# Performance work log

Measured on AMD Instinct MI355X. Metric: run time of the kernel, lower is better.

## Reference

```python
import jax, jax.numpy as jnp
import numpy as np

EMBED_DIM = 768
NUM_HEADS = 8
HEAD_DIM = EMBED_DIM // NUM_HEADS
SCALE = HEAD_DIM ** -0.5
B = 256
N_TOTAL = 16384


def setup_inputs() -> dict:
    key = jax.random.key(0)
    ks = jax.random.split(key, 10)
    s = 1.0 / np.sqrt(EMBED_DIM)
    inp = {
        "query": jax.random.normal(ks[0], (B, EMBED_DIM), jnp.float32),
        "search": jax.random.normal(ks[1], (N_TOTAL, EMBED_DIM), jnp.float32),
        # q_proj / k_proj: Linear(embed_dim, embed_dim)
        "Wq": jax.random.uniform(ks[2], (EMBED_DIM, EMBED_DIM), jnp.float32, -s, s),
        "bq": jax.random.uniform(ks[3], (EMBED_DIM,), jnp.float32, -s, s),
        "Wk": jax.random.uniform(ks[4], (EMBED_DIM, EMBED_DIM), jnp.float32, -s, s),
        "bk": jax.random.uniform(ks[5], (EMBED_DIM,), jnp.float32, -s, s),
        # score_fusion: Linear(H, H//2) -> GELU -> Linear(H//2, 1)
        "W1": jax.random.uniform(ks[6], (NUM_HEADS // 2, NUM_HEADS), jnp.float32, -1.0 / np.sqrt(NUM_HEADS), 1.0 / np.sqrt(NUM_HEADS)),
        "b1": jax.random.uniform(ks[7], (NUM_HEADS // 2,), jnp.float32, -1.0 / np.sqrt(NUM_HEADS), 1.0 / np.sqrt(NUM_HEADS)),
        "W2": jax.random.uniform(ks[8], (1, NUM_HEADS // 2), jnp.float32, -1.0 / np.sqrt(NUM_HEADS // 2), 1.0 / np.sqrt(NUM_HEADS // 2)),
        "b2": jax.random.uniform(ks[9], (1,), jnp.float32, -1.0 / np.sqrt(NUM_HEADS // 2), 1.0 / np.sqrt(NUM_HEADS // 2)),
    }
    return inp


def reference(query, search, Wq, bq, Wk, bk, W1, b1, W2, b2):
    Bq = query.shape[0]
    Nt = search.shape[0]
    # projections -> (B, H, hd) and (N, H, hd)
    q = (query @ Wq.T + bq).reshape(Bq, NUM_HEADS, HEAD_DIM)
    k = (search @ Wk.T + bk).reshape(Nt, NUM_HEADS, HEAD_DIM)
    # per-head dot products: (B, N, H)
    attn_logits = jnp.einsum('bhd,nhd->bnh', q, k) * SCALE
    # tiny MLP over head axis: H -> H//2 -> 1, exact (erf) GELU as in torch default
    h = jax.nn.gelu(attn_logits @ W1.T + b1, approximate=False)
    scores = h @ W2.T + b2  # (B, N, 1)
    return scores.squeeze(-1)
```

## Files before the change

### kernel.cpp

```cpp
#include <hip/hip_runtime.h>
#include <math.h>

#define SCALE 0.1020620726159658f

typedef __attribute__((ext_vector_type(8))) short shortx8;
typedef __attribute__((ext_vector_type(4))) float floatx4;

__device__ __forceinline__ unsigned short f2bf(float f) {
  union { float f; unsigned int i; } c; c.f = f;
  unsigned int x = c.i;
  x += 0x7fffu + ((x >> 16) & 1u);
  return (unsigned short)(x >> 16);
}
__device__ __forceinline__ float gelu_fast(float x) {
  float x2 = x * x;
  float y = x * (0.7978845608f + 0.0356774081f * x2);
  float e = fminf(y * 2.885390082f, 60.0f);
  float t = exp2f(e);
  return x * t * __builtin_amdgcn_rcpf(t + 1.0f);
}
__device__ __forceinline__ void async_ld16(const unsigned short* g, unsigned short* l) {
  __builtin_amdgcn_global_load_lds(
      (const __attribute__((address_space(1))) unsigned int*)g,
      (__attribute__((address_space(3))) unsigned int*)l, 16, 0, 0);
}
__device__ __forceinline__ void cvt_store8(const float* __restrict__ src,
                                           unsigned short* __restrict__ dst) {
  float4 a = *(const float4*)src;
  float4 b = *(const float4*)(src + 4);
  shortx8 v;
  v[0] = (short)f2bf(a.x); v[1] = (short)f2bf(a.y);
  v[2] = (short)f2bf(a.z); v[3] = (short)f2bf(a.w);
  v[4] = (short)f2bf(b.x); v[5] = (short)f2bf(b.y);
  v[6] = (short)f2bf(b.z); v[7] = (short)f2bf(b.w);
  *(shortx8*)dst = v;
}
__device__ __forceinline__ void mfma_consume(const unsigned short* __restrict__ As,
                                             const unsigned short* __restrict__ Bs,
                                             int wr, int wc, int quad, int l15,
                                             floatx4 (&acc)[4][4]) {
#pragma unroll
  for (int ks = 0; ks < 2; ks++) {
    shortx8 af[4], bfr[4];
#pragma unroll
    for (int mt = 0; mt < 4; mt++) {
      int r = wr * 64 + mt * 16 + l15;
      int ch = (ks * 4 + quad) ^ (r & 7);
      af[mt] = *(const shortx8*)(As + r * 64 + ch * 8);
    }
#pragma unroll
    for (int nt = 0; nt < 4; nt++) {
      int r = wc * 64 + nt * 16 + l15;
      int ch = (ks * 4 + quad) ^ (r & 7);
      bfr[nt] = *(const shortx8*)(Bs + r * 64 + ch * 8);
    }
#pragma unroll
    for (int mt = 0; mt < 4; mt++)
#pragma unroll
      for (int nt = 0; nt < 4; nt++)
        acc[mt][nt] = __builtin_amdgcn_mfma_f32_16x16x32_bf16(
            af[mt], bfr[nt], acc[mt][nt], 0, 0, 0);
  }
}

__global__ __launch_bounds__(256) void k_pre(
    const float* __restrict__ query, const float* __restrict__ Wq,
    const float* __restrict__ bq, const float* __restrict__ W1,
    const float* __restrict__ Wk, const float* __restrict__ search,
    float* __restrict__ qf, unsigned short* __restrict__ QW,
    unsigned short* __restrict__ WkT, unsigned short* __restrict__ sb,
    int use_sb)
{
  __shared__ unsigned short As[64 * 64];
  __shared__ unsigned short Bs[64 * 64];
  __shared__ unsigned short tile[32][33];
  const int bid = blockIdx.x, t = threadIdx.x;
  const int wave = t >> 6, lane = t & 63;
  if (bid < 48) {
    const int by = bid / 12, bx = bid % 12;
    const int m0 = by * 64, n0 = bx * 64;
    const int wr = wave >> 1, wc = wave & 1;
    const int quad = lane >> 4, l15 = lane & 15;
    const int rl = lane >> 3, cL = lane & 7, p = cL ^ rl;
    floatx4 acc[2][2];
#pragma unroll
    for (int i = 0; i < 2; i++)
#pragma unroll
      for (int j = 0; j < 2; j++) acc[i][j] = (floatx4){0.f, 0.f, 0.f, 0.f};
    for (int k0 = 0; k0 < 768; k0 += 64) {
#pragma unroll
      for (int tt = 0; tt < 2; tt++) {
        int r = wave * 16 + tt * 8 + rl;
        cvt_store8(query + (size_t)(m0 + r) * 768 + k0 + cL * 8, As + r * 64 + p * 8);
        cvt_store8(Wq + (size_t)(n0 + r) * 768 + k0 + cL * 8, Bs + r * 64 + p * 8);
      }
      __syncthreads();
#pragma unroll
      for (int ks = 0; ks < 2; ks++) {
        shortx8 af[2], bfr[2];
#pragma unroll
        for (int mt = 0; mt < 2; mt++) {
          int r = wr * 32 + mt * 16 + l15;
          int ch = (ks * 4 + quad) ^ (r & 7);
          af[mt] = *(const shortx8*)(As + r * 64 + ch * 8);
        }
#pragma unroll
        for (int nt = 0; nt < 2; nt++) {
          int r = wc * 32 + nt * 16 + l15;
          int ch = (ks * 4 + quad) ^ (r & 7);
          bfr[nt] = *(const shortx8*)(Bs + r * 64 + ch * 8);
        }
#pragma unroll
        for (int mt = 0; mt < 2; mt++)
#pragma unroll
          for (int nt = 0; nt < 2; nt++)
            acc[mt][nt] = __builtin_amdgcn_mfma_f32_16x16x32_bf16(
                af[mt], bfr[nt], acc[mt][nt], 0, 0, 0);
      }
      __syncthreads();
    }
    const int lrow = quad * 4;
#pragma unroll
    for (int mt = 0; mt < 2; mt++)
#pragma unroll
      for (int nt = 0; nt < 2; nt++) {
        int gm = m0 + wr * 32 + mt * 16 + lrow;
        int gn = n0 + wc * 32 + nt * 16 + l15;
        float bz = bq[gn];
        int h = gn / 96;
        float w1h0 = W1[h], w1h1 = W1[8 + h], w1h2 = W1[16 + h], w1h3 = W1[24 + h];
#pragma unroll
        for (int r = 0; r < 4; r++) {
          float qv = acc[mt][nt][r] + bz;
          qf[(size_t)(gm + r) * 768 + gn] = qv;
          size_t base = (size_t)((gm + r) * 4) * 768 + gn;
          QW[base]           = f2bf(SCALE * w1h0 * qv);
          QW[base + 768]     = f2bf(SCALE * w1h1 * qv);
          QW[base + 2 * 768] = f2bf(SCALE * w1h2 * qv);
          QW[base + 3 * 768] = f2bf(SCALE * w1h3 * qv);
        }
      }
  } else if (bid < 624) {
    const int tb = bid - 48, bx = tb % 24, by = tb / 24;
    const int tx = t & 31, ty = t >> 5;
#pragma unroll
    for (int i = 0; i < 4; i++)
      tile[ty + i * 8][tx] = f2bf(Wk[(size_t)(by * 32 + ty + i * 8) * 768 + bx * 32 + tx]);
    __syncthreads();
#pragma unroll
    for (int i = 0; i < 4; i++)
      WkT[(size_t)(bx * 32 + ty + i * 8) * 768 + by * 32 + tx] = tile[tx][ty + i * 8];
  } else {
    for (int it = bid - 624; it < 6144; it += 1000) {
      size_t i = (size_t)it * 2048 + t * 8;
      cvt_store8(search + i, sb + i);
    }
  }
}

__global__ __launch_bounds__(256) void k_mid(
    const unsigned short* __restrict__ QW, const unsigned short* __restrict__ WkT,
    unsigned short* __restrict__ QQ,
    const float* __restrict__ qf, const float* __restrict__ W1,
    const float* __restrict__ b1, const float* __restrict__ bk,
    float* __restrict__ cp)
{
  __shared__ unsigned short As[64 * 64];
  __shared__ unsigned short Bs[64 * 64];
  const int bid = blockIdx.x, t = threadIdx.x;
  const int wave = t >> 6, lane = t & 63;
  if (bid < 192) {
    const int by = bid / 12, bx = bid % 12;
    const int m0 = by * 64, n0 = bx * 64;
    const int wr = wave >> 1, wc = wave & 1;
    const int quad = lane >> 4, l15 = lane & 15;
    const int rl = lane >> 3, cl = (lane & 7) ^ rl;
    floatx4 acc[2][2];
#pragma unroll
    for (int i = 0; i < 2; i++)
#pragma unroll
      for (int j = 0; j < 2; j++) acc[i][j] = (floatx4){0.f, 0.f, 0.f, 0.f};
    for (int k0 = 0; k0 < 768; k0 += 64) {
#pragma unroll
      for (int tt = 0; tt < 2; tt++) {
        int rr = wave * 16 + tt * 8;
        async_ld16(QW + (size_t)(m0 + rr + rl) * 768 + k0 + cl * 8, As + rr * 64);
        async_ld16(WkT + (size_t)(n0 + rr + rl) * 768 + k0 + cl * 8, Bs + rr * 64);
      }
      __syncthreads();
#pragma unroll
      for (int ks = 0; ks < 2; ks++) {
        shortx8 af[2], bfr[2];
#pragma unroll
        for (int mt = 0; mt < 2; mt++) {
          int r = wr * 32 + mt * 16 + l15;
          int ch = (ks * 4 + quad) ^ (r & 7);
          af[mt] = *(const shortx8*)(As + r * 64 + ch * 8);
        }
#pragma unroll
        for (int nt = 0; nt < 2; nt++) {
          int r = wc * 32 + nt * 16 + l15;
          int ch = (ks * 4 + quad) ^ (r & 7);
          bfr[nt] = *(const shortx8*)(Bs + r * 64 + ch * 8);
        }
#pragma unroll
        for (int mt = 0; mt < 2; mt++)
#pragma unroll
          for (int nt = 0; nt < 2; nt++)
            acc[mt][nt] = __builtin_amdgcn_mfma_f32_16x16x32_bf16(
                af[mt], bfr[nt], acc[mt][nt], 0, 0, 0);
      }
      __syncthreads();
    }
    const int lrow = quad * 4;
#pragma unroll
    for (int mt = 0; mt < 2; mt++)
#pragma unroll
      for (int nt = 0; nt < 2; nt++) {
        int gm = m0 + wr * 32 + mt * 16 + lrow;
        int gn = n0 + wc * 32 + nt * 16 + l15;
#pragma unroll
        for (int r = 0; r < 4; r++)
          QQ[(size_t)(gm + r) * 768 + gn] = f2bf(acc[mt][nt][r]);
      }
  } else {
    const int bstart = (bid - 192) * 64;
    for (int b = bstart + wave; b < bstart + 64; b += 4) {
      const float* qrow = qf + (size_t)b * 768;
      int e0 = lane * 12;
      float s = 0.f;
#pragma unroll
      for (int i = 0; i < 12; i++) s += qrow[e0 + i] * bk[e0 + i];
      s += __shfl_xor(s, 1); s += __shfl_xor(s, 2); s += __shfl_xor(s, 4);
      float v = __shfl(s, (lane & 7) * 8);
      float w = W1[((lane >> 3) & 3) * 8 + (lane & 7)] * v;
      w += __shfl_xor(w, 1); w += __shfl_xor(w, 2); w += __shfl_xor(w, 4);
      if (lane < 32 && (lane & 7) == 0) {
        int j = lane >> 3;
        cp[b * 4 + j] = b1[j] + SCALE * w;
      }
    }
  }
}

__global__ __launch_bounds__(256) void k_main(
    const unsigned short* __restrict__ QQ, const void* __restrict__ Bv,
    float* __restrict__ out, const float* __restrict__ cp,
    const float* __restrict__ W2, const float* __restrict__ b2, int use_sb)
{
  __shared__ unsigned short As[128 * 64];
  __shared__ unsigned short Bs[128 * 64];
  const int bid = blockIdx.x;
  const int n_tile = (bid & 7) * 16 + ((bid >> 3) & 15);
  const int m_tile = bid >> 7;
  const int m0 = m_tile * 128, n0 = n_tile * 128;
  const int t = threadIdx.x, wave = t >> 6, lane = t & 63;
  const int wr = wave >> 1, wc = wave & 1;
  const int quad = lane >> 4, l15 = lane & 15;
  floatx4 acc[4][4];
#pragma unroll
  for (int i = 0; i < 4; i++)
#pragma unroll
    for (int j = 0; j < 4; j++) acc[i][j] = (floatx4){0.f, 0.f, 0.f, 0.f};
  const int rl = lane >> 3, cl = (lane & 7) ^ rl, cL = lane & 7, p = cL ^ rl;
  for (int k0 = 0; k0 < 768; k0 += 64) {
#pragma unroll
    for (int tt = 0; tt < 4; tt++) {
      int rr = wave * 32 + tt * 8;
      async_ld16(QQ + (size_t)(m0 + rr + rl) * 768 + k0 + cl * 8, As + rr * 64);
    }
    if (use_sb) {
      const unsigned short* B16 = (const unsigned short*)Bv;
#pragma unroll
      for (int tt = 0; tt < 4; tt++) {
        int rr = wave * 32 + tt * 8;
        async_ld16(B16 + (size_t)(n0 + rr + rl) * 768 + k0 + cl * 8, Bs + rr * 64);
      }
    } else {
      const float* Bf = (const float*)Bv;
#pragma unroll
      for (int tt = 0; tt < 4; tt++) {
        int r = wave * 32 + tt * 8 + rl;
        cvt_store8(Bf + (size_t)(n0 + r) * 768 + k0 + cL * 8, Bs + r * 64 + p * 8);
      }
    }
    __syncthreads();
    mfma_consume(As, Bs, wr, wc, quad, l15, acc);
    __syncthreads();
  }
  const float w2v0 = W2[0], w2v1 = W2[1], w2v2 = W2[2], w2v3 = W2[3];
  const float b2v = b2[0];
  const int lrow = quad * 4;
#pragma unroll
  for (int mt = 0; mt < 4; mt++) {
    int gm = m0 + wr * 64 + mt * 16 + lrow;
    float cpv0 = cp[gm], cpv1 = cp[gm + 1], cpv2 = cp[gm + 2], cpv3 = cp[gm + 3];
#pragma unroll
    for (int nt = 0; nt < 4; nt++) {
      int gn = n0 + wc * 64 + nt * 16 + l15;
      floatx4 v = acc[mt][nt];
      float s = b2v;
      s += w2v0 * gelu_fast(v[0] + cpv0);
      s += w2v1 * gelu_fast(v[1] + cpv1);
      s += w2v2 * gelu_fast(v[2] + cpv2);
      s += w2v3 * gelu_fast(v[3] + cpv3);
      out[(size_t)(gm >> 2) * 16384 + gn] = s;
    }
  }
}

extern "C" void kernel_launch(void* const* d_in, const int* in_sizes, int n_in,
                              void* d_out, int out_size, void* d_ws, size_t ws_size,
                              hipStream_t stream) {
  const float* query  = (const float*)d_in[0];
  const float* search = (const float*)d_in[1];
  const float* Wq     = (const float*)d_in[2];
  const float* bq     = (const float*)d_in[3];
  const float* Wk     = (const float*)d_in[4];
  const float* bk     = (const float*)d_in[5];
  const float* W1     = (const float*)d_in[6];
  const float* b1     = (const float*)d_in[7];
  const float* W2     = (const float*)d_in[8];
  const float* b2     = (const float*)d_in[9];
  float* out = (float*)d_out;

  char* ws = (char*)d_ws;
  float*          cp  = (float*)ws;
  float*          qf  = (float*)(ws + 4352);
  unsigned short* WkT = (unsigned short*)(ws + 790784);
  unsigned short* QW  = (unsigned short*)(ws + 1970432);
  unsigned short* QQ  = (unsigned short*)(ws + 3543296);
  unsigned short* sb  = (unsigned short*)(ws + 5116160);
  int use_sb = (ws_size >= 30281984u) ? 1 : 0;

  k_pre<<<use_sb ? 1624 : 624, 256, 0, stream>>>(query, Wq, bq, W1, Wk, search,
                                                 qf, QW, WkT, sb, use_sb);
  k_mid<<<196, 256, 0, stream>>>(QW, WkT, QQ, qf, W1, b1, bk, cp);
  k_main<<<1024, 256, 0, stream>>>(QQ, use_sb ? (const void*)sb : (const void*)search,
                                   out, cp, W2, b2, use_sb);
}
```

Before: 167.9 us.

## Merge mid-stage GEMM into prologue kernel using atomic counter dependency

```diff
diff --git a/kernel.cpp b/kernel.cpp
--- a/kernel.cpp
+++ b/kernel.cpp
@@ -67,9 +67,11 @@
     const float* __restrict__ query, const float* __restrict__ Wq,
     const float* __restrict__ bq, const float* __restrict__ W1,
     const float* __restrict__ Wk, const float* __restrict__ search,
+    const float* __restrict__ b1, const float* __restrict__ bk,
     float* __restrict__ qf, unsigned short* __restrict__ QW,
     unsigned short* __restrict__ WkT, unsigned short* __restrict__ sb,
-    int use_sb)
+    unsigned short* __restrict__ QQ, float* __restrict__ cp,
+    unsigned int* __restrict__ ctr, int use_sb)
 {
   __shared__ unsigned short As[64 * 64];
   __shared__ unsigned short Bs[64 * 64];
@@ -140,6 +142,11 @@
           QW[base + 3 * 768] = f2bf(SCALE * w1h3 * qv);
         }
       }
+    __syncthreads();
+    if (t == 0) {
+      __threadfence();
+      __hip_atomic_fetch_add(ctr, 1u, __ATOMIC_RELEASE, __HIP_MEMORY_SCOPE_AGENT);
+    }
   } else if (bid < 624) {
     const int tb = bid - 48, bx = tb % 24, by = tb / 24;
     const int tx = t & 31, ty = t >> 5;
@@ -150,94 +157,98 @@
 #pragma unroll
     for (int i = 0; i < 4; i++)
       WkT[(size_t)(bx * 32 + ty + i * 8) * 768 + by * 32 + tx] = tile[tx][ty + i * 8];
+    __syncthreads();
+    if (t == 0) {
+      __threadfence();
+      __hip_atomic_fetch_add(ctr, 1u, __ATOMIC_RELEASE, __HIP_MEMORY_SCOPE_AGENT);
+    }
+  } else if (use_sb && bid < 1648) {
+    const int fid = bid - 624;
+    const int x = fid & 7, idx = fid >> 3;
+    const size_t base = ((size_t)(2048 * x + 16 * idx)) * 768;
+#pragma unroll
+    for (int j = 0; j < 6; j++) {
+      size_t i = base + j * 2048 + t * 8;
+      cvt_store8(search + i, sb + i);
+    }
   } else {
-    for (int it = bid - 624; it < 6144; it += 1000) {
-      size_t i = (size_t)it * 2048 + t * 8;
-      cvt_store8(search + i, sb + i);
-    }
-  }
-}
-
-__global__ __launch_bounds__(256) void k_mid(
-    const unsigned short* __restrict__ QW, const unsigned short* __restrict__ WkT,
-    unsigned short* __restrict__ QQ,
-    const float* __restrict__ qf, const float* __restrict__ W1,
-    const float* __restrict__ b1, const float* __restrict__ bk,
-    float* __restrict__ cp)
-{
-  __shared__ unsigned short As[64 * 64];
-  __shared__ unsigned short Bs[64 * 64];
-  const int bid = blockIdx.x, t = threadIdx.x;
-  const int wave = t >> 6, lane = t & 63;
-  if (bid < 192) {
-    const int by = bid / 12, bx = bid % 12;
-    const int m0 = by * 64, n0 = bx * 64;
-    const int wr = wave >> 1, wc = wave & 1;
-    const int quad = lane >> 4, l15 = lane & 15;
-    const int rl = lane >> 3, cl = (lane & 7) ^ rl;
-    floatx4 acc[2][2];
-#pragma unroll
-    for (int i = 0; i < 2; i++)
-#pragma unroll
-      for (int j = 0; j < 2; j++) acc[i][j] = (floatx4){0.f, 0.f, 0.f, 0.f};
-    for (int k0 = 0; k0 < 768; k0 += 64) {
-#pragma unroll
-      for (int tt = 0; tt < 2; tt++) {
-        int rr = wave * 16 + tt * 8;
-        async_ld16(QW + (size_t)(m0 + rr + rl) * 768 + k0 + cl * 8, As + rr * 64);
-        async_ld16(WkT + (size_t)(n0 + rr + rl) * 768 + k0 + cl * 8, Bs + rr * 64);
-      }
-      __syncthreads();
-#pragma unroll
-      for (int ks = 0; ks < 2; ks++) {
-        shortx8 af[2], bfr[2];
-#pragma unroll
-        for (int mt = 0; mt < 2; mt++) {
-          int r = wr * 32 + mt * 16 + l15;
-          int ch = (ks * 4 + quad) ^ (r & 7);
-          af[mt] = *(const shortx8*)(As + r * 64 + ch * 8);
-        }
+    const int cid = bid - (use_sb ? 1648 : 624);
+    if (t == 0) {
+      while (__hip_atomic_load(ctr, __ATOMIC_ACQUIRE, __HIP_MEMORY_SCOPE_AGENT) < 624u)
+        __builtin_amdgcn_s_sleep(8);
+      __threadfence();
+    }
+    __syncthreads();
+    if (cid < 192) {
+      const int by = cid / 12, bx = cid % 12;
+      const int m0 = by * 64, n0 = bx * 64;
+      const int wr = wave >> 1, wc = wave & 1;
+      const int quad = lane >> 4, l15 = lane & 15;
+      const int rl = lane >> 3, cl = (lane & 7) ^ rl;
+      floatx4 acc[2][2];
+#pragma unroll
+      for (int i = 0; i < 2; i++)
+#pragma unroll
+        for (int j = 0; j < 2; j++) acc[i][j] = (floatx4){0.f, 0.f, 0.f, 0.f};
+      for (int k0 = 0; k0 < 768; k0 += 64) {
+#pragma unroll
+        for (int tt = 0; tt < 2; tt++) {
+          int rr = wave * 16 + tt * 8;
+          async_ld16(QW + (size_t)(m0 + rr + rl) * 768 + k0 + cl * 8, As + rr * 64);
+          async_ld16(WkT + (size_t)(n0 + rr + rl) * 768 + k0 + cl * 8, Bs + rr * 64);
+        }
+        __syncthreads();
+#pragma unroll
+        for (int ks = 0; ks < 2; ks++) {
+          shortx8 af[2], bfr[2];
+#pragma unroll
+          for (int mt = 0; mt < 2; mt++) {
+            int r = wr * 32 + mt * 16 + l15;
+            int ch = (ks * 4 + quad) ^ (r & 7);
+            af[mt] = *(const shortx8*)(As + r * 64 + ch * 8);
+          }
+#pragma unroll
+          for (int nt = 0; nt < 2; nt++) {
+            int r = wc * 32 + nt * 16 + l15;
+            int ch = (ks * 4 + quad) ^ (r & 7);
+            bfr[nt] = *(const shortx8*)(Bs + r * 64 + ch * 8);
+          }
+#pragma unroll
+          for (int mt = 0; mt < 2; mt++)
+#pragma unroll
+            for (int nt = 0; nt < 2; nt++)
+              acc[mt][nt] = __builtin_amdgcn_mfma_f32_16x16x32_bf16(
+                  af[mt], bfr[nt], acc[mt][nt], 0, 0, 0);
+        }
+        __syncthreads();
+      }
+      const int lrow = quad * 4;
+#pragma unroll
+      for (int mt = 0; mt < 2; mt++)
 #pragma unroll
         for (int nt = 0; nt < 2; nt++) {
-          int r = wc * 32 + nt * 16 + l15;
-          int ch = (ks * 4 + quad) ^ (r & 7);
-          bfr[nt] = *(const shortx8*)(Bs + r * 64 + ch * 8);
-        }
-#pragma unroll
-        for (int mt = 0; mt < 2; mt++)
-#pragma unroll
-          for (int nt = 0; nt < 2; nt++)
-            acc[mt][nt] = __builtin_amdgcn_mfma_f32_16x16x32_bf16(
-                af[mt], bfr[nt], acc[mt][nt], 0, 0, 0);
-      }
-      __syncthreads();
-    }
-    const int lrow = quad * 4;
-#pragma unroll
-    for (int mt = 0; mt < 2; mt++)
-#pragma unroll
-      for (int nt = 0; nt < 2; nt++) {
-        int gm = m0 + wr * 32 + mt * 16 + lrow;
-        int gn = n0 + wc * 32 + nt * 16 + l15;
-#pragma unroll
-        for (int r = 0; r < 4; r++)
-          QQ[(size_t)(gm + r) * 768 + gn] = f2bf(acc[mt][nt][r]);
-      }
-  } else {
-    const int bstart = (bid - 192) * 64;
-    for (int b = bstart + wave; b < bstart + 64; b += 4) {
-      const float* qrow = qf + (size_t)b * 768;
-      int e0 = lane * 12;
-      float s = 0.f;
-#pragma unroll
-      for (int i = 0; i < 12; i++) s += qrow[e0 + i] * bk[e0 + i];
-      s += __shfl_xor(s, 1); s += __shfl_xor(s, 2); s += __shfl_xor(s, 4);
-      float v = __shfl(s, (lane & 7) * 8);
-      float w = W1[((lane >> 3) & 3) * 8 + (lane & 7)] * v;
-      w += __shfl_xor(w, 1); w += __shfl_xor(w, 2); w += __shfl_xor(w, 4);
-      if (lane < 32 && (lane & 7) == 0) {
-        int j = lane >> 3;
-        cp[b * 4 + j] = b1[j] + SCALE * w;
+          int gm = m0 + wr * 32 + mt * 16 + lrow;
+          int gn = n0 + wc * 32 + nt * 16 + l15;
+#pragma unroll
+          for (int r = 0; r < 4; r++)
+            QQ[(size_t)(gm + r) * 768 + gn] = f2bf(acc[mt][nt][r]);
+        }
+    } else {
+      const int bstart = (cid - 192) * 64;
+      for (int b = bstart + wave; b < bstart + 64; b += 4) {
+        const float* qrow = qf + (size_t)b * 768;
+        int e0 = lane * 12;
+        float s = 0.f;
+#pragma unroll
+        for (int i = 0; i < 12; i++) s += qrow[e0 + i] * bk[e0 + i];
+        s += __shfl_xor(s, 1); s += __shfl_xor(s, 2); s += __shfl_xor(s, 4);
+        float v = __shfl(s, (lane & 7) * 8);
+        float w = W1[((lane >> 3) & 3) * 8 + (lane & 7)] * v;
+        w += __shfl_xor(w, 1); w += __shfl_xor(w, 2); w += __shfl_xor(w, 4);
+        if (lane < 32 && (lane & 7) == 0) {
+          int j = lane >> 3;
+          cp[b * 4 + j] = b1[j] + SCALE * w;
+        }
       }
     }
   }
@@ -325,17 +336,19 @@
   float* out = (float*)d_out;
 
   char* ws = (char*)d_ws;
-  float*          cp  = (float*)ws;
-  float*          qf  = (float*)(ws + 4352);
-  unsigned short* WkT = (unsigned short*)(ws + 790784);
-  unsigned short* QW  = (unsigned short*)(ws + 1970432);
-  unsigned short* QQ  = (unsigned short*)(ws + 3543296);
-  unsigned short* sb  = (unsigned short*)(ws + 5116160);
-  int use_sb = (ws_size >= 30281984u) ? 1 : 0;
-
-  k_pre<<<use_sb ? 1624 : 624, 256, 0, stream>>>(query, Wq, bq, W1, Wk, search,
-                                                 qf, QW, WkT, sb, use_sb);
-  k_mid<<<196, 256, 0, stream>>>(QW, WkT, QQ, qf, W1, b1, bk, cp);
+  unsigned int*   ctr = (unsigned int*)ws;
+  float*          cp  = (float*)(ws + 4096);
+  float*          qf  = (float*)(ws + 8448);
+  unsigned short* WkT = (unsigned short*)(ws + 794880);
+  unsigned short* QW  = (unsigned short*)(ws + 1974528);
+  unsigned short* QQ  = (unsigned short*)(ws + 3547392);
+  unsigned short* sb  = (unsigned short*)(ws + 5120256);
+  int use_sb = (ws_size >= 30286080u) ? 1 : 0;
+
+  hipMemsetAsync(ctr, 0, 64, stream);
+  k_pre<<<use_sb ? 1844 : 820, 256, 0, stream>>>(query, Wq, bq, W1, Wk, search,
+                                                 b1, bk, qf, QW, WkT, sb, QQ, cp,
+                                                 ctr, use_sb);
   k_main<<<1024, 256, 0, stream>>>(QQ, use_sb ? (const void*)sb : (const void*)search,
                                    out, cp, W2, b2, use_sb);
 }
```

After: 250.6 us. +49.3%, slower.
